# Optimization experiments

Hardware: AMD Instinct MI355X
Metric: run time of the kernel (lower is better)

Reference implementation:

```python
import jax, jax.numpy as jnp
import numpy as np

EPS = 1e-8
EPS12 = 1e-12
TAU = 0.2
IOU_THRESHOLD = 0.5
NEG_INF = -1e9

N, C = 8192, 1024
HID, FGD, CLSD = 256, 64, 128


def setup_inputs() -> dict:
    key = jax.random.key(0)
    ks = jax.random.split(key, 16)
    roi_feats = jax.random.normal(ks[0], (N, C), dtype=jnp.float32)
    # labels in {-1 (ignore), 0 (bg), 1..20 (classes)}
    labels = jax.random.randint(ks[1], (N,), 0, 21, dtype=jnp.int64) - 1
    ious = jax.random.uniform(ks[2], (N,), dtype=jnp.float32)
    s = 0.02
    w1f = jax.random.normal(ks[3], (HID, C), dtype=jnp.float32) * s
    b1f = jnp.zeros((HID,), dtype=jnp.float32)
    w2f = jax.random.normal(ks[4], (FGD, HID), dtype=jnp.float32) * s
    b2f = jnp.zeros((FGD,), dtype=jnp.float32)
    w1c = jax.random.normal(ks[5], (HID, C), dtype=jnp.float32) * s
    b1c = jnp.zeros((HID,), dtype=jnp.float32)
    w2c = jax.random.normal(ks[6], (CLSD, HID), dtype=jnp.float32) * s
    b2c = jnp.zeros((CLSD,), dtype=jnp.float32)
    return {"roi_feats": roi_feats, "labels": labels, "ious": ious,
            "w1f": w1f, "b1f": b1f, "w2f": w2f, "b2f": b2f,
            "w1c": w1c, "b1c": b1c, "w2c": w2c, "b2c": b2c}


def _project_normalize(x, w1, b1, w2, b2):
    h = jax.nn.relu(x @ w1.T + b1)
    z = h @ w2.T + b2
    nrm = jnp.linalg.norm(z, axis=1, keepdims=True)  # F.normalize: z / max(||z||, eps)
    return z / jnp.maximum(nrm, EPS)


def _fg_bg_loss(z_fg, fg_mask, ignore_mask, iou_weight):
    n = z_fg.shape[0]
    anchor = fg_mask & ~ignore_mask
    eye = jnp.eye(n, dtype=bool)
    # pos_mask[i,j] = fg_mask[j] & ~ignore[j], self excluded
    pos = (fg_mask & ~ignore_mask)[None, :] & ~eye  # [N,N]
    sim = (z_fg @ z_fg.T) / TAU
    sim_exp = jnp.exp(sim) * (~eye).astype(sim.dtype)
    denom = sim_exp.sum(axis=1)  # [N]
    numer = jnp.sum(jnp.exp(sim) * pos.astype(sim.dtype), axis=1)  # [N]
    n_pos = pos.sum(axis=1)
    loss_i = -jnp.log((numer + EPS) / (denom + EPS))
    valid = anchor & (n_pos > 0)
    w = iou_weight
    num = jnp.sum(jnp.where(valid, loss_i * w, 0.0))
    den = jnp.sum(jnp.where(valid, w, 0.0)) + EPS
    return num / den


def _class_supcon_loss(z_cls, labels, fg_mask, ignore_mask, iou_weight):
    n = z_cls.shape[0]
    anchor = fg_mask & ~ignore_mask
    eye = jnp.eye(n, dtype=bool)
    valid_den = ~eye & ~ignore_mask[None, :]  # [N,N]
    # pos[i,j]: same label, j not ignored, labels[j] != 0, j != i, j valid
    pos = (labels[None, :] == labels[:, None]) & ~ignore_mask[None, :] & (labels[None, :] != 0)
    pos = pos & ~eye & valid_den
    sim = (z_cls @ z_cls.T) / TAU
    logits = jnp.where(valid_den, sim, NEG_INF)
    denom_log = jax.nn.logsumexp(logits, axis=1)  # [N]
    n_pos = pos.sum(axis=1)
    sum_pos = jnp.sum(jnp.where(pos, sim, 0.0), axis=1)
    n_pos_safe = jnp.maximum(n_pos, 1).astype(sim.dtype)
    loss_i = -(sum_pos - n_pos.astype(sim.dtype) * denom_log) / n_pos_safe
    valid = anchor & (n_pos > 0) & valid_den.any(axis=1)
    w = iou_weight
    num = jnp.sum(jnp.where(valid, loss_i * w, 0.0))
    den = jnp.sum(jnp.where(valid, w, 0.0)) + EPS12
    return num / den


def reference(roi_feats, labels, ious, w1f, b1f, w2f, b2f, w1c, b1c, w2c, b2c):
    z_fg = _project_normalize(roi_feats, w1f, b1f, w2f, b2f)
    z_cls = _project_normalize(roi_feats, w1c, b1c, w2c, b2c)
    ignore_mask = labels == -1
    bg_mask = (labels == 0) & ~ignore_mask
    fg_mask = (labels > 0) & ~ignore_mask
    iou_weight = jnp.where(ious > IOU_THRESHOLD, ious, 0.0)
    loss_fg_bg = _fg_bg_loss(z_fg, fg_mask, ignore_mask, iou_weight)
    loss_supcon = _class_supcon_loss(z_cls, labels, fg_mask, ignore_mask, iou_weight)
    # loss_weights = (1.0, 1.0); stacked as [loss_fg_bg, loss_supcon]
    return jnp.stack([loss_fg_bg * 1.0, loss_supcon * 1.0])
```

## Files before the change

kernel.cpp:

```cpp
#include <hip/hip_runtime.h>
#include <hip/hip_bf16.h>
#include <math.h>

#define N_ROI 8192
#define C_IN  1024
#define HIDD  256
#define FGD   64
#define CLSD  128
#define INV_TAU 5.0f
#define SCALE_LOG2E 7.2134752f
#define LN2F 0.69314718f

using frag_ab = __attribute__((ext_vector_type(8))) short;
using f32x16  = __attribute__((ext_vector_type(16))) float;

static __device__ __forceinline__ short f32_to_bf16_bits(float f) {
  unsigned u = __builtin_bit_cast(unsigned, f);
  u = (u + 0x7FFFu + ((u >> 16) & 1u)) >> 16;
  return (short)u;
}
static __device__ __forceinline__ float bf16_bits_to_f32(short b) {
  unsigned u = ((unsigned)(unsigned short)b) << 16;
  return __builtin_bit_cast(float, u);
}
static __device__ __forceinline__ float fast_exp2(float x) {
#if __has_builtin(__builtin_amdgcn_exp2f)
  return __builtin_amdgcn_exp2f(x);
#else
  return exp2f(x);
#endif
}
static __device__ __forceinline__ void async_copy16(const short* g, short* l) {
  __builtin_amdgcn_global_load_lds(
      (const __attribute__((address_space(1))) unsigned int*)g,
      (__attribute__((address_space(3))) unsigned int*)l, 16, 0, 0);
}

__global__ __launch_bounds__(256) void pack_zero_kernel(
    const float* __restrict__ w1f, const float* __restrict__ w1c,
    const float* __restrict__ w2f, const float* __restrict__ w2c,
    short* __restrict__ W1pf, short* __restrict__ W1pc,
    short* __restrict__ W2pf, short* __restrict__ W2pc,
    float* __restrict__ accum, int* __restrict__ cnt) {
  int b = blockIdx.x;
  if (b == 280) {
    int t = threadIdx.x;
    if (t < 8) accum[t] = 0.f;
    if (t < 24) cnt[t] = 0;
    return;
  }
  const float* src; short* dst; int Ksh; int b0;
  if (b < 128)      { src = w1f; dst = W1pf; Ksh = 10; b0 = 0; }
  else if (b < 256) { src = w1c; dst = W1pc; Ksh = 10; b0 = 128; }
  else if (b < 264) { src = w2f; dst = W2pf; Ksh = 8;  b0 = 256; }
  else              { src = w2c; dst = W2pc; Ksh = 8;  b0 = 264; }
  int K = 1 << Ksh;
  int f = (b - b0) * 256 + threadIdx.x;
  int r = f >> (Ksh - 3);
  int c0 = (f & ((K >> 3) - 1)) << 3;
  float4 v0 = *(const float4*)(src + (size_t)r * K + c0);
  float4 v1 = *(const float4*)(src + (size_t)r * K + c0 + 4);
  union { short s[8]; uint4 v; } o;
  o.s[0] = f32_to_bf16_bits(v0.x); o.s[1] = f32_to_bf16_bits(v0.y);
  o.s[2] = f32_to_bf16_bits(v0.z); o.s[3] = f32_to_bf16_bits(v0.w);
  o.s[4] = f32_to_bf16_bits(v1.x); o.s[5] = f32_to_bf16_bits(v1.y);
  o.s[6] = f32_to_bf16_bits(v1.z); o.s[7] = f32_to_bf16_bits(v1.w);
  ((uint4*)dst)[(size_t)((r >> 5) * (K >> 4) + (c0 >> 4)) * 64 +
                ((c0 >> 3) & 1) * 32 + (r & 31)] = o.v;
}

template<int D>
__device__ __forceinline__ void gemm2_from_lds(
    const short* __restrict__ T2,
    const short* __restrict__ W2p, const float* __restrict__ b2,
    short* __restrict__ Zr, float* __restrict__ tii,
    short* __restrict__ T, int gt) {
  int lane = threadIdx.x & 63;
  const frag_ab* Wv = (const frag_ab*)W2p;
  constexpr int NT = D / 32;
  frag_ab a[16];
  #pragma unroll
  for (int kc = 0; kc < 16; ++kc)
    a[kc] = *(const frag_ab*)&T2[(lane & 31) * 264 + kc * 16 + (lane >> 5) * 8];
  f32x16 acc[NT];
  #pragma unroll
  for (int j = 0; j < NT; ++j)
    #pragma unroll
    for (int q = 0; q < 16; ++q) acc[j][q] = 0.f;
  #pragma unroll
  for (int kc = 0; kc < 16; ++kc)
    #pragma unroll
    for (int j = 0; j < NT; ++j)
      acc[j] = __builtin_amdgcn_mfma_f32_32x32x16_bf16(a[kc], Wv[(j * 16 + kc) * 64 + lane], acc[j], 0, 0, 0);
  int c = lane & 31, h = lane >> 5;
  float bb[NT];
  #pragma unroll
  for (int j = 0; j < NT; ++j) bb[j] = b2[j * 32 + c];
  float s1[16];
  #pragma unroll
  for (int r = 0; r < 16; ++r) {
    s1[r] = 0.f;
    #pragma unroll
    for (int j = 0; j < NT; ++j) {
      float v = acc[j][r] + bb[j];
      s1[r] += v * v;
    }
  }
  #pragma unroll
  for (int r = 0; r < 16; ++r)
    #pragma unroll
    for (int m = 1; m < 32; m <<= 1) s1[r] += __shfl_xor(s1[r], m);
  float s2[16];
  #pragma unroll
  for (int r = 0; r < 16; ++r) s2[r] = 0.f;
  #pragma unroll
  for (int j = 0; j < NT; ++j) {
    int cl = j * 32 + c;
    #pragma unroll
    for (int g = 0; g < 4; ++g) {
      short q0, q1, q2, q3;
      #pragma unroll
      for (int e = 0; e < 4; ++e) {
        int r = g * 4 + e;
        float sc = 1.f / fmaxf(sqrtf(s1[r]), 1e-8f);
        short qb = f32_to_bf16_bits((acc[j][r] + bb[j]) * sc);
        float zf = bf16_bits_to_f32(qb);
        s2[r] += zf * zf;
        if (e == 0) q0 = qb; else if (e == 1) q1 = qb; else if (e == 2) q2 = qb; else q3 = qb;
      }
      *(short4*)&T[cl * 36 + 4 * h + 8 * g] = make_short4(q0, q1, q2, q3);
    }
  }
  #pragma unroll
  for (int r = 0; r < 16; ++r)
    #pragma unroll
    for (int m = 1; m < 32; m <<= 1) s2[r] += __shfl_xor(s2[r], m);
  if (c == 0) {
    #pragma unroll
    for (int r = 0; r < 16; ++r)
      tii[gt * 32 + (r & 3) + 8 * (r >> 2) + 4 * h] = s2[r];
  }
  uint4* Zv = (uint4*)Zr;
  #pragma unroll
  for (int k = 0; k < D / 16; ++k) {
    int c0 = (2 * k + h) * 8;
    union { short s[8]; uint4 u; } o;
    #pragma unroll
    for (int e = 0; e < 8; ++e) o.s[e] = T[(c0 + e) * 36 + c];
    Zv[(size_t)(gt * (D / 16) + k) * 64 + h * 32 + c] = o.u;
  }
}

__global__ __launch_bounds__(256) void fused_mlp_kernel(
    const float* __restrict__ X,
    const short* __restrict__ W1pf, const short* __restrict__ W1pc,
    const float* __restrict__ b1f, const float* __restrict__ b1c,
    const short* __restrict__ W2pf, const short* __restrict__ W2pc,
    const float* __restrict__ b2f, const float* __restrict__ b2c,
    short* __restrict__ Zrf, short* __restrict__ Zrc,
    float* __restrict__ tiif, float* __restrict__ tiic,
    const int* __restrict__ labels,
    float* __restrict__ Sfg, float* __restrict__ Pfg,
    float* __restrict__ Scls, float* __restrict__ SPc,
    float* __restrict__ pfv, float* __restrict__ nimv,
    float* __restrict__ ljmv, int* __restrict__ cnt) {
  __shared__ short stageA[2][1024];
  __shared__ short T2[32 * 264];
  __shared__ short Tw[128 * 36];
  int tid = threadIdx.x, lane = tid & 63, wv = tid >> 6;
  int Mb = blockIdx.x, head = blockIdx.y;

  if (head == 0 && tid < 32) {
    int i = Mb * 32 + tid;
    Sfg[i] = 0.f; Pfg[i] = 0.f; Scls[i] = 0.f; SPc[i] = 0.f;
    int l = labels[i];
    pfv[i]  = (l > 0)  ? 1.f : 0.f;
    nimv[i] = (l != -1) ? 1.f : 0.f;
    ljmv[i] = (l > 0)  ? (float)l : -7.f;
    int b = l + 1; if (b < 0) b = 0; if (b > 21) b = 21;
    atomicAdd(&cnt[b], 1);
  }

  const short* Wp = head ? W1pc : W1pf;
  const float* b1 = head ? b1c  : b1f;
  const uint4* Wv4 = (const uint4*)Wp;
  int arow = tid >> 3;
  int ac4  = tid & 7;
  const float* Xp = X + (size_t)(Mb * 32 + arow) * C_IN + ac4 * 4;
  int aslot = ((ac4 >> 2) * 64 + ((ac4 >> 1) & 1) * 32 + arow) * 8 + (ac4 & 1) * 4;

  float4 av;
  frag_ab breg[2][4];
  f32x16 acc[2];
  #pragma unroll
  for (int nt = 0; nt < 2; ++nt)
    #pragma unroll
    for (int q = 0; q < 16; ++q) acc[nt][q] = 0.f;

  auto loadA = [&](int c) { av = *(const float4*)(Xp + c * 32); };
  auto loadB = [&](int c, int s) {
    #pragma unroll
    for (int kci = 0; kci < 2; ++kci)
      #pragma unroll
      for (int nt = 0; nt < 2; ++nt)
        breg[s][kci * 2 + nt] =
            *(const frag_ab*)&Wv4[(size_t)((wv * 2 + nt) * 64 + c * 2 + kci) * 64 + lane];
  };
  auto storeA = [&](int buf) {
    *(short4*)&stageA[buf][aslot] =
        make_short4(f32_to_bf16_bits(av.x), f32_to_bf16_bits(av.y),
                    f32_to_bf16_bits(av.z), f32_to_bf16_bits(av.w));
  };
  auto domfma = [&](int buf, int bank) {
    frag_ab a0 = *(const frag_ab*)&stageA[buf][(0 * 64 + lane) * 8];
    frag_ab a1 = *(const frag_ab*)&stageA[buf][(1 * 64 + lane) * 8];
    #pragma unroll
    for (int nt = 0; nt < 2; ++nt)
      acc[nt] = __builtin_amdgcn_mfma_f32_32x32x16_bf16(a0, breg[bank][nt], acc[nt], 0, 0, 0);
    #pragma unroll
    for (int nt = 0; nt < 2; ++nt)
      acc[nt] = __builtin_amdgcn_mfma_f32_32x32x16_bf16(a1, breg[bank][2 + nt], acc[nt], 0, 0, 0);
  };

  loadA(0); loadB(0, 0); storeA(0);
  __syncthreads();
  for (int c = 0; c < 32; c += 2) {
    if (c + 1 < 32) { loadA(c + 1); loadB(c + 1, 1); }
    domfma(0, 0);
    if (c + 1 < 32) storeA(1);
    __syncthreads();
    if (c + 2 < 32) { loadA(c + 2); loadB(c + 2, 0); }
    domfma(1, 1);
    if (c + 2 < 32) storeA(0);
    __syncthreads();
  }
  {
    int cl31 = lane & 31, h = lane >> 5;
    #pragma unroll
    for (int nt = 0; nt < 2; ++nt) {
      int gc = wv * 64 + nt * 32 + cl31;
      float bb = b1[gc];
      #pragma unroll
      for (int q = 0; q < 16; ++q) {
        int row = (q & 3) + 8 * (q >> 2) + 4 * h;
        float x = fmaxf(acc[nt][q] + bb, 0.f);
        T2[row * 264 + gc] = f32_to_bf16_bits(x);
      }
    }
  }
  __syncthreads();

  if (wv == 0) {
    if (head == 0)
      gemm2_from_lds<FGD>(T2, W2pf, b2f, Zrf, tiif, Tw, Mb);
    else
      gemm2_from_lds<CLSD>(T2, W2pc, b2c, Zrc, tiic, Tw, Mb);
  }
}

template<int D, int MODE, int NJT>
__device__ __forceinline__ void loss_body(
    const short* __restrict__ Zr, const int* __restrict__ labels,
    const float* __restrict__ pfv, const float* __restrict__ nimv,
    const float* __restrict__ ljmv,
    float* __restrict__ Sg, float* __restrict__ Pg,
    short* __restrict__ jbuf) {
  constexpr int KC = D / 16;
  constexpr int TSH = KC * 64 * 8;
  constexpr int LD = (KC * 64) / 256;
  int tid = threadIdx.x, lane = tid & 63, wv = tid >> 6;
  int itile = (blockIdx.x >> 1) * 4 + wv;
  const frag_ab* Zrv = (const frag_ab*)Zr;
  frag_ab a[KC];
  #pragma unroll
  for (int kc = 0; kc < KC; ++kc) {
    frag_ab t = Zrv[(itile * KC + kc) * 64 + lane];
    #pragma unroll
    for (int e = 0; e < 8; ++e)
      t[e] = f32_to_bf16_bits(bf16_bits_to_f32(t[e]) * SCALE_LOG2E);
    a[kc] = t;
  }
  float limf[16];
  if (MODE == 1) {
    #pragma unroll
    for (int r = 0; r < 16; ++r) {
      int row = (r & 3) + 8 * (r >> 2) + 4 * (lane >> 5);
      limf[r] = (float)labels[itile * 32 + row];
    }
  }
  float Ssum[16] = {}, Psum[16] = {};
  int jt0 = blockIdx.y * NJT;
  int jlane = lane & 31;

  auto STAGE = [&](short* dst, int kk) {
    const short* src = Zr + (size_t)(jt0 + kk) * KC * 512;
    #pragma unroll
    for (int u = 0; u < LD; ++u)
      async_copy16(src + (size_t)(u * 256 + tid) * 8,
                   dst + (u * 256 + (wv * 64)) * 8);
  };

  STAGE(jbuf, 0);
  asm volatile("s_waitcnt vmcnt(0)" ::: "memory");
  __builtin_amdgcn_s_barrier();
  short* cur = jbuf; short* nxt = jbuf + TSH;

  for (int kk = 0; kk < NJT; ++kk) {
    if (kk + 1 < NJT) STAGE(nxt, kk + 1);
    int j = (jt0 + kk) * 32 + jlane;
    float pf = 0.f, nim = 0.f, ljm = 0.f;
    if (MODE == 0) pf = pfv[j];
    else { nim = nimv[j]; ljm = ljmv[j]; }
    f32x16 acc;
    #pragma unroll
    for (int q = 0; q < 16; ++q) acc[q] = 0.f;
    __builtin_amdgcn_s_setprio(1);
    #pragma unroll
    for (int kc = 0; kc < KC; ++kc) {
      frag_ab b = *(const frag_ab*)&cur[(kc * 64 + lane) * 8];
      acc = __builtin_amdgcn_mfma_f32_32x32x16_bf16(a[kc], b, acc, 0, 0, 0);
    }
    __builtin_amdgcn_s_setprio(0);
    #pragma unroll
    for (int rr = 0; rr < 16; ++rr) {
      float e = fast_exp2(acc[rr]);
      if (MODE == 0) {
        Ssum[rr] += e;
        Psum[rr] = fmaf(pf, e, Psum[rr]);
      } else {
        Ssum[rr] = fmaf(nim, e, Ssum[rr]);
        Psum[rr] += (limf[rr] == ljm) ? acc[rr] : 0.f;
      }
    }
    asm volatile("s_waitcnt vmcnt(0)" ::: "memory");
    __builtin_amdgcn_s_barrier();
    short* t = cur; cur = nxt; nxt = t;
  }

  #pragma unroll
  for (int r = 0; r < 16; ++r) {
    float s = Ssum[r], p = Psum[r];
    #pragma unroll
    for (int m = 1; m < 32; m <<= 1) { s += __shfl_xor(s, m); p += __shfl_xor(p, m); }
    if ((lane & 31) == 0) {
      if (MODE == 1) p *= LN2F;
      int row = (r & 3) + 8 * (r >> 2) + 4 * (lane >> 5);
      atomicAdd(&Sg[itile * 32 + row], s);
      atomicAdd(&Pg[itile * 32 + row], p);
    }
  }
}

__global__ __launch_bounds__(256, 4) void loss_kernel(
    const short* __restrict__ Zrf, const short* __restrict__ Zrc,
    const int* __restrict__ labels,
    const float* __restrict__ pfv, const float* __restrict__ nimv,
    const float* __restrict__ ljmv,
    float* __restrict__ Sfg, float* __restrict__ Pfg,
    float* __restrict__ Scls, float* __restrict__ SPc) {
  __shared__ short jbuf[2 * 8 * 64 * 8];
  if ((blockIdx.x & 1) == 0)
    loss_body<FGD, 0, 16>(Zrf, labels, pfv, nimv, ljmv, Sfg, Pfg, jbuf);
  else
    loss_body<CLSD, 1, 16>(Zrc, labels, pfv, nimv, ljmv, Scls, SPc, jbuf);
}

__global__ __launch_bounds__(256) void finalize_kernel(
    const float* __restrict__ Sfg, const float* __restrict__ Pfg,
    const float* __restrict__ Scls, const float* __restrict__ SPc,
    const float* __restrict__ tiif, const float* __restrict__ tiic,
    const int* __restrict__ labels, const float* __restrict__ ious,
    int* __restrict__ cnt, float* __restrict__ accum, float* __restrict__ out) {
  int i = blockIdx.x * 256 + threadIdx.x;
  int l = labels[i];
  float iv = ious[i];
  float w = (iv > 0.5f) ? iv : 0.f;
  int cntP = 0;
  #pragma unroll
  for (int b = 2; b <= 21; ++b) cntP += cnt[b];
  int cntNI = N_ROI - cnt[0];
  bool Pi = (l > 0);
  float numF = 0.f, denF = 0.f, numC = 0.f, denC = 0.f;
  float eF = __expf(INV_TAU * tiif[i]);
  float Sf = Sfg[i] - eF;
  float Pf = Pfg[i] - (Pi ? eF : 0.f);
  int nposF = cntP - (Pi ? 1 : 0);
  if (Pi && nposF > 0) {
    float lossF = logf((Sf + 1e-8f) / (Pf + 1e-8f));
    numF = lossF * w; denF = w;
  }
  float tC = INV_TAU * tiic[i];
  float eC = __expf(tC);
  float Sc = Scls[i] - ((l != -1) ? eC : 0.f);
  float SP = SPc[i] - (Pi ? tC : 0.f);
  int nposC = Pi ? (cnt[l + 1] - 1) : 0;
  bool anyv = (cntNI - ((l != -1) ? 1 : 0)) > 0;
  if (Pi && nposC > 0 && anyv) {
    float lse = logf(Sc);
    float lossC = -(SP - (float)nposC * lse) / fmaxf((float)nposC, 1.f);
    numC = lossC * w; denC = w;
  }
  float v0 = numF, v1 = denF, v2 = numC, v3 = denC;
  #pragma unroll
  for (int m = 1; m < 64; m <<= 1) {
    v0 += __shfl_xor(v0, m); v1 += __shfl_xor(v1, m);
    v2 += __shfl_xor(v2, m); v3 += __shfl_xor(v3, m);
  }
  __shared__ float red[4][4];
  int lane = threadIdx.x & 63, wid = threadIdx.x >> 6;
  if (lane == 0) { red[wid][0]=v0; red[wid][1]=v1; red[wid][2]=v2; red[wid][3]=v3; }
  __syncthreads();
  if (threadIdx.x == 0) {
    float s0=0,s1=0,s2=0,s3=0;
    for (int q = 0; q < 4; ++q) { s0+=red[q][0]; s1+=red[q][1]; s2+=red[q][2]; s3+=red[q][3]; }
    atomicAdd(&accum[0], s0); atomicAdd(&accum[1], s1);
    atomicAdd(&accum[2], s2); atomicAdd(&accum[3], s3);
    __threadfence();
    int t = atomicAdd(&cnt[22], 1);
    if (t == 31) {
      __threadfence();
      out[0] = accum[0] / (accum[1] + 1e-8f);
      out[1] = accum[2] / (accum[3] + 1e-12f);
    }
  }
}

extern "C" void kernel_launch(void* const* d_in, const int* in_sizes, int n_in,
                              void* d_out, int out_size, void* d_ws, size_t ws_size,
                              hipStream_t stream) {
  const float* X    = (const float*)d_in[0];
  const int*  labels= (const int*)d_in[1];
  const float* ious = (const float*)d_in[2];
  const float* w1f  = (const float*)d_in[3];
  const float* b1f  = (const float*)d_in[4];
  const float* w2f  = (const float*)d_in[5];
  const float* b2f  = (const float*)d_in[6];
  const float* w1c  = (const float*)d_in[7];
  const float* b1c  = (const float*)d_in[8];
  const float* w2c  = (const float*)d_in[9];
  const float* b2c  = (const float*)d_in[10];
  float* out = (float*)d_out;

  char* w = (char*)d_ws;
  short* W1pf = (short*)w;            w += 524288;
  short* W1pc = (short*)w;            w += 524288;
  short* W2pf = (short*)w;            w += 32768;
  short* W2pc = (short*)w;            w += 65536;
  short* Zrf  = (short*)w;            w += 1048576;
  short* Zrc  = (short*)w;            w += 2097152;
  float* Sfg  = (float*)w;            w += 32768;
  float* Pfg  = (float*)w;            w += 32768;
  float* Scls = (float*)w;            w += 32768;
  float* SPc  = (float*)w;            w += 32768;
  float* tiif = (float*)w;            w += 32768;
  float* tiic = (float*)w;            w += 32768;
  float* pfv  = (float*)w;            w += 32768;
  float* nimv = (float*)w;            w += 32768;
  float* ljmv = (float*)w;            w += 32768;
  float* accum= (float*)w;            w += 32;
  int*   cnt  = (int*)w;              w += 96;

  pack_zero_kernel<<<281, 256, 0, stream>>>(w1f, w1c, w2f, w2c,
                                            W1pf, W1pc, W2pf, W2pc, accum, cnt);

  fused_mlp_kernel<<<dim3(256, 2), 256, 0, stream>>>(X, W1pf, W1pc, b1f, b1c,
                                            W2pf, W2pc, b2f, b2c,
                                            Zrf, Zrc, tiif, tiic,
                                            labels, Sfg, Pfg, Scls, SPc,
                                            pfv, nimv, ljmv, cnt);

  loss_kernel<<<dim3(128, 16), 256, 0, stream>>>(Zrf, Zrc, labels, pfv, nimv, ljmv,
                                                 Sfg, Pfg, Scls, SPc);

  finalize_kernel<<<N_ROI/256, 256, 0, stream>>>(Sfg, Pfg, Scls, SPc, tiif, tiic,
                                                 labels, ious, cnt, accum, out);
}
```

Before: 188.2 us.

## Triple-buffer j-tile staging and prefetch per-column masks into LDS

The loss kernel moves from double-buffered LDS staging with a full vmcnt(0) wait after every tile to a three-buffer ring. Each step waits only on the oldest outstanding load, so two tiles stay in flight. The per-column mask vectors (pf, nim, ljm) for the block's whole j-range are also loaded into LDS asynchronously up front, replacing a global load on every iteration. This raises LDS use per block and relies on hand-counted vmcnt values that must match the number of issued async copies.

```diff
diff --git a/kernel.cpp b/kernel.cpp
--- a/kernel.cpp
+++ b/kernel.cpp
@@ -30,7 +30,7 @@
   return exp2f(x);
 #endif
 }
-static __device__ __forceinline__ void async_copy16(const short* g, short* l) {
+static __device__ __forceinline__ void async_copy16(const void* g, void* l) {
   __builtin_amdgcn_global_load_lds(
       (const __attribute__((address_space(1))) unsigned int*)g,
       (__attribute__((address_space(3))) unsigned int*)l, 16, 0, 0);
@@ -264,13 +264,16 @@
     const float* __restrict__ pfv, const float* __restrict__ nimv,
     const float* __restrict__ ljmv,
     float* __restrict__ Sg, float* __restrict__ Pg,
-    short* __restrict__ jbuf) {
+    short* __restrict__ smem) {
   constexpr int KC = D / 16;
   constexpr int TSH = KC * 64 * 8;
   constexpr int LD = (KC * 64) / 256;
   int tid = threadIdx.x, lane = tid & 63, wv = tid >> 6;
   int itile = (blockIdx.x >> 1) * 4 + wv;
+  int jt0 = blockIdx.y * NJT;
+  int jlane = lane & 31;
   const frag_ab* Zrv = (const frag_ab*)Zr;
+
   frag_ab a[KC];
   #pragma unroll
   for (int kc = 0; kc < KC; ++kc) {
@@ -288,9 +291,22 @@
       limf[r] = (float)labels[itile * 32 + row];
     }
   }
-  float Ssum[16] = {}, Psum[16] = {};
-  int jt0 = blockIdx.y * NJT;
-  int jlane = lane & 31;
+  asm volatile("s_waitcnt vmcnt(0)" ::: "memory");
+
+  short* b0 = smem;
+  short* b1 = smem + TSH;
+  short* b2 = smem + 2 * TSH;
+  float* maskf = (float*)(smem + 3 * TSH);
+
+  if (MODE == 0) {
+    if (tid < 128)
+      async_copy16(pfv + jt0 * 32 + tid * 4, maskf + wv * 256);
+  } else {
+    if (tid < 128)
+      async_copy16(nimv + jt0 * 32 + tid * 4, maskf + wv * 256);
+    else
+      async_copy16(ljmv + jt0 * 32 + (tid - 128) * 4, maskf + 512 + (wv - 2) * 256);
+  }
 
   auto STAGE = [&](short* dst, int kk) {
     const short* src = Zr + (size_t)(jt0 + kk) * KC * 512;
@@ -300,24 +316,33 @@
                    dst + (u * 256 + (wv * 64)) * 8);
   };
 
-  STAGE(jbuf, 0);
-  asm volatile("s_waitcnt vmcnt(0)" ::: "memory");
-  __builtin_amdgcn_s_barrier();
-  short* cur = jbuf; short* nxt = jbuf + TSH;
-
-  for (int kk = 0; kk < NJT; ++kk) {
-    if (kk + 1 < NJT) STAGE(nxt, kk + 1);
-    int j = (jt0 + kk) * 32 + jlane;
+  STAGE(b0, 0); STAGE(b1, 1);
+
+  float Ssum[16] = {}, Psum[16] = {};
+
+  #pragma unroll 1
+  for (int t = 0; t < NJT; ++t) {
+    if (t < NJT - 1) {
+      if (LD == 1) asm volatile("s_waitcnt vmcnt(1)" ::: "memory");
+      else         asm volatile("s_waitcnt vmcnt(2)" ::: "memory");
+    } else {
+      asm volatile("s_waitcnt vmcnt(0)" ::: "memory");
+    }
+    __builtin_amdgcn_s_barrier();
+    __builtin_amdgcn_sched_barrier(0);
+    if (t + 2 < NJT) STAGE(b2, t + 2);
+
     float pf = 0.f, nim = 0.f, ljm = 0.f;
-    if (MODE == 0) pf = pfv[j];
-    else { nim = nimv[j]; ljm = ljmv[j]; }
+    if (MODE == 0) pf = maskf[t * 32 + jlane];
+    else { nim = maskf[t * 32 + jlane]; ljm = maskf[512 + t * 32 + jlane]; }
+
     f32x16 acc;
     #pragma unroll
     for (int q = 0; q < 16; ++q) acc[q] = 0.f;
     __builtin_amdgcn_s_setprio(1);
     #pragma unroll
     for (int kc = 0; kc < KC; ++kc) {
-      frag_ab b = *(const frag_ab*)&cur[(kc * 64 + lane) * 8];
+      frag_ab b = *(const frag_ab*)&b0[(kc * 64 + lane) * 8];
       acc = __builtin_amdgcn_mfma_f32_32x32x16_bf16(a[kc], b, acc, 0, 0, 0);
     }
     __builtin_amdgcn_s_setprio(0);
@@ -332,9 +357,7 @@
         Psum[rr] += (limf[rr] == ljm) ? acc[rr] : 0.f;
       }
     }
-    asm volatile("s_waitcnt vmcnt(0)" ::: "memory");
-    __builtin_amdgcn_s_barrier();
-    short* t = cur; cur = nxt; nxt = t;
+    short* tmp = b0; b0 = b1; b1 = b2; b2 = tmp;
   }
 
   #pragma unroll
@@ -358,11 +381,11 @@
     const float* __restrict__ ljmv,
     float* __restrict__ Sfg, float* __restrict__ Pfg,
     float* __restrict__ Scls, float* __restrict__ SPc) {
-  __shared__ short jbuf[2 * 8 * 64 * 8];
+  __shared__ short smem[3 * 8 * 64 * 8 + 2048];
   if ((blockIdx.x & 1) == 0)
-    loss_body<FGD, 0, 16>(Zrf, labels, pfv, nimv, ljmv, Sfg, Pfg, jbuf);
+    loss_body<FGD, 0, 16>(Zrf, labels, pfv, nimv, ljmv, Sfg, Pfg, smem);
   else
-    loss_body<CLSD, 1, 16>(Zrc, labels, pfv, nimv, ljmv, Scls, SPc, jbuf);
+    loss_body<CLSD, 1, 16>(Zrc, labels, pfv, nimv, ljmv, Scls, SPc, smem);
 }
 
 __global__ __launch_bounds__(256) void finalize_kernel(
```

Measured after the change: 187.9 us. About the same (-0.2%).
